# Optimization experiments

Measured on AMD Instinct MI355X. Metric: run time of the kernel, lower is better.

The kernel has to match this reference:

```python
import jax, jax.numpy as jnp
import numpy as np

B, LC, LE, H, V = 128, 256, 257, 512, 128
PAD = 0  # padding_token_index


def lstm_cell(x, h, c, Wih, Whh, b):
    # torch LSTMCell gate order: i, f, g, o
    g = x @ Wih.T + h @ Whh.T + b
    i, f, gg, o = jnp.split(g, 4, axis=-1)
    c = jax.nn.sigmoid(f) * c + jax.nn.sigmoid(i) * jnp.tanh(gg)
    h = jax.nn.sigmoid(o) * jnp.tanh(c)
    return h, c


def setup_inputs() -> dict:
    key = jax.random.key(0)
    ks = jax.random.split(key, 32)
    p = lambda k, shape: jax.random.normal(k, shape, jnp.float32) * 0.05
    d = {
        'C_idx': jax.random.randint(ks[0], (B, LC), 0, V, dtype=jnp.int32),
        'E_idx': jax.random.randint(ks[1], (B, LE), 0, V, dtype=jnp.int32),
        'C_pad': jnp.zeros((B, LC), dtype=bool),
        'enc_Wih_f': p(ks[2], (4 * H, V)),
        'enc_Whh_f': p(ks[3], (4 * H, H)),
        'enc_b_f': p(ks[4], (4 * H,)),
        'enc_Wih_b': p(ks[5], (4 * H, V)),
        'enc_Whh_b': p(ks[6], (4 * H, H)),
        'enc_b_b': p(ks[7], (4 * H,)),
        'dec_Wih': p(ks[8], (4 * H, H + V)),
        'dec_Whh': p(ks[9], (4 * H, H)),
        'dec_b': p(ks[10], (4 * H,)),
        'Wh': p(ks[11], (H, 2 * H)),
        'Wc': p(ks[12], (H, 2 * H)),
        'Wattn': p(ks[13], (H, 2 * H)),
        'Wout': p(ks[14], (H, 3 * H)),
        'Wvocab': p(ks[15], (V, H)),
        'pg_ctx': p(ks[16], (2 * H,)),
        'pg_in': p(ks[17], (V + H,)),
        'pg_h': p(ks[18], (H,)),
        'pg_c': p(ks[19], (H,)),
        'pg_b': p(ks[20], (1,)),
    }
    return d


def _forward(C_idx, E_idx, C_pad, enc_Wih_f, enc_Whh_f, enc_b_f, enc_Wih_b, enc_Whh_b, enc_b_b,
             dec_Wih, dec_Whh, dec_b, Wh, Wc, Wattn, Wout, Wvocab,
             pg_ctx, pg_in, pg_h, pg_c, pg_b):
    C = jax.nn.one_hot(C_idx, V, dtype=jnp.float32)      # [B,LC,V]
    E_emb = jax.nn.one_hot(E_idx, V, dtype=jnp.float32)  # [B,LE,V]
    z = jnp.zeros((B, H), jnp.float32)

    xs = jnp.swapaxes(C, 0, 1)  # [LC,B,V]

    def enc_fwd(carry, x):
        h, c = lstm_cell(x, carry[0], carry[1], enc_Wih_f, enc_Whh_f, enc_b_f)
        return (h, c), h

    def enc_bwd(carry, x):
        h, c = lstm_cell(x, carry[0], carry[1], enc_Wih_b, enc_Whh_b, enc_b_b)
        return (h, c), h

    (hf, cf), Hf = jax.lax.scan(enc_fwd, (z, z), xs)
    (hb, cb), Hb = jax.lax.scan(enc_bwd, (z, z), xs[::-1])
    Hb = Hb[::-1]
    enc = jnp.swapaxes(jnp.concatenate([Hf, Hb], axis=-1), 0, 1)  # [B,LC,2H]

    # decoder init state from final encoder states (fwd;bwd concat)
    h0 = jnp.concatenate([hf, hb], axis=-1) @ Wh.T
    c0 = jnp.concatenate([cf, cb], axis=-1) @ Wc.T

    enc_proj = enc @ Wattn.T  # [B,LC,H]

    def step(carry, x_emb):
        h, c, prev_out = carry
        nin = jnp.concatenate([x_emb, prev_out], axis=1)  # [B,V+H]
        h, c = lstm_cell(nin, h, c, dec_Wih, dec_Whh, dec_b)
        scores = jnp.einsum('blh,bh->bl', enc_proj, h)
        scores = jnp.where(C_pad, -jnp.inf, scores)
        attn = jax.nn.softmax(scores, axis=1)             # [B,LC]
        ctx = jnp.einsum('bl,blh->bh', attn, enc)         # [B,2H]
        t_out = jnp.tanh(jnp.concatenate([h, ctx], axis=1) @ Wout.T)  # [B,H]
        gen = jax.nn.softmax(t_out @ Wvocab.T, axis=1)    # [B,V]
        p_gen = jax.nn.sigmoid(ctx @ pg_ctx + nin @ pg_in + h @ pg_h + c @ pg_c + pg_b[0])[:, None]
        copy_p = attn * (1.0 - p_gen)
        out = jax.vmap(lambda o, idx, a: o.at[idx].add(a))(gen * p_gen, C_idx, copy_p)
        return (h, c, t_out), out

    xs2 = jnp.swapaxes(E_emb[:, :LE - 1], 0, 1)  # teacher inputs, step 0 = start token
    _, preds = jax.lax.scan(step, (h0, c0, z), xs2)
    preds = jnp.swapaxes(preds, 0, 1)  # [B,LE-1,V]

    tgt = E_idx[:, 1:]
    nll = -jnp.take_along_axis(jnp.log(preds), tgt[..., None], axis=2)[..., 0]
    return jnp.where(tgt == PAD, 0.0, nll)  # [B,LE-1], reduction='none'


def reference(C_idx, E_idx, C_pad, enc_Wih_f, enc_Whh_f, enc_b_f, enc_Wih_b, enc_Whh_b, enc_b_b,
              dec_Wih, dec_Whh, dec_b, Wh, Wc, Wattn, Wout, Wvocab,
              pg_ctx, pg_in, pg_h, pg_c, pg_b):
    return _forward(C_idx, E_idx, C_pad, enc_Wih_f, enc_Whh_f, enc_b_f, enc_Wih_b, enc_Whh_b, enc_b_b,
                    dec_Wih, dec_Whh, dec_b, Wh, Wc, Wattn, Wout, Wvocab,
                    pg_ctx, pg_in, pg_h, pg_c, pg_b)
```

## Files before the change

### kernel.cpp

```cpp
#include <hip/hip_runtime.h>

static constexpr size_t OFF_ENC   = 0;
static constexpr size_t OFF_WGE   = 67108864;
static constexpr size_t OFF_WIHTE = 71303168;
static constexpr size_t OFF_HENC  = 72351744;
static constexpr size_t OFF_CENC  = 72876032;
static constexpr size_t OFF_WGATE = 67108864;
static constexpr size_t OFF_XDEC  = 71303168;
static constexpr size_t OFF_WATTT = 71827456;
static constexpr size_t OFF_WOUT  = 72876032;
static constexpr size_t OFF_WVOCT = 74448896;
static constexpr size_t OFF_HDEC  = 74579968;
static constexpr size_t OFF_CDEC  = 74842112;
static constexpr size_t OFF_TOUT  = 75104256;
static constexpr size_t OFF_UFB   = 75366400;
static constexpr size_t OFF_CTXF  = 75628544;
static constexpr size_t OFF_CTXP  = 75890688;
static constexpr size_t OFF_SC    = 76414976;
static constexpr size_t OFF_MSP   = 76480512;
static constexpr size_t OFF_MD    = 76482560;

__device__ __forceinline__ float sigm(float x) { return 1.f / (1.f + expf(-x)); }
__device__ __forceinline__ unsigned short f2bf(float f) {
  unsigned u = __float_as_uint(f);
  u += 0x7fffu + ((u >> 16) & 1u);
  return (unsigned short)(u >> 16);
}
__device__ __forceinline__ float bfl(unsigned w) { return __uint_as_float(w << 16); }
__device__ __forceinline__ float bfh(unsigned w) { return __uint_as_float(w & 0xffff0000u); }
__device__ __forceinline__ float bf2f(unsigned short v) { return __uint_as_float(((unsigned)v) << 16); }

#if defined(__has_builtin)
#if __has_builtin(__builtin_amdgcn_fdot2_f32_bf16)
#define HAVE_DOT2BF 1
#endif
#endif
#ifdef HAVE_DOT2BF
typedef __bf16 bf2_t __attribute__((ext_vector_type(2)));
__device__ __forceinline__ float dot2bf(unsigned w, unsigned h, float acc) {
  return __builtin_amdgcn_fdot2_f32_bf16(__builtin_bit_cast(bf2_t, w),
                                         __builtin_bit_cast(bf2_t, h), acc, false);
}
#else
__device__ __forceinline__ float dot2bf(unsigned w, unsigned h, float acc) {
  return acc + bfl(w) * bfl(h) + bfh(w) * bfh(h);
}
#endif

__global__ __launch_bounds__(256) void k_pre1(const float* __restrict__ WhhF,
                                              const float* __restrict__ WhhB,
                                              const float* __restrict__ WihF,
                                              const float* __restrict__ WihB,
                                              char* __restrict__ wsb) {
  unsigned short* dst = (unsigned short*)(wsb + OFF_WGE);
  int id = blockIdx.x * 256 + threadIdx.x, str = gridDim.x * 256;
  for (int x = id; x < 2097152; x += str) {
    int dir = x >> 20, r = x & 1048575;
    int e = r & 7, j = (r >> 3) & 511, k2 = r >> 12;
    int g = e >> 1, k = k2 * 2 + (e & 1);
    const float* W = dir ? WhhB : WhhF;
    dst[x] = f2bf(W[((size_t)g * 512 + j) * 512 + k]);
  }
  for (int x = id; x < 524288; x += str) {
    int dir = x >> 18, r = x & 262143;
    int g = r & 3, j = (r >> 2) & 511, v = r >> 11;
    const float* W = dir ? WihB : WihF;
    dst[2097152 + x] = f2bf(W[((size_t)g * 512 + j) * 128 + v]);
  }
}

__global__ __launch_bounds__(512) void k_enc(const float* __restrict__ bF,
                                             const float* __restrict__ bB,
                                             const int* __restrict__ C_idx,
                                             char* __restrict__ wsb) {
  __shared__ __align__(16) unsigned short hbf[512];
  int bid = blockIdx.x;
  int b = bid & 127, dir = bid >> 7;
  int j = threadIdx.x;
  const unsigned short* WH = (const unsigned short*)(wsb + OFF_WGE) + (size_t)dir * 1048576;
  const unsigned short* WX = (const unsigned short*)(wsb + OFF_WGE) + 2097152 + (size_t)dir * 262144;
  const float* bias = dir ? bB : bF;
  float b0 = bias[j], b1 = bias[512 + j], b2 = bias[1024 + j], b3 = bias[1536 + j];
  unsigned short* encb = (unsigned short*)wsb + (size_t)b * 262144;
  const uint4* wp = (const uint4*)WH + j;
  float c = 0.f, h = 0.f;
  hbf[j] = 0;
  __syncthreads();
  for (int t = 0; t < 256; ++t) {
    int l = dir ? (255 - t) : t;
    int cidx = C_idx[b * 256 + l];
    uint2 xg = *(const uint2*)(WX + ((size_t)cidx * 512 + j) * 4);
    float a0 = b0 + bfl(xg.x), a1 = b1 + bfh(xg.x);
    float a2 = b2 + bfl(xg.y), a3 = b3 + bfh(xg.y);
    for (int k2 = 0; k2 < 256; ++k2) {
      uint4 w = wp[(size_t)k2 * 512];
      unsigned hp = *(const unsigned*)((const char*)hbf + k2 * 4);
      a0 = dot2bf(w.x, hp, a0);
      a1 = dot2bf(w.y, hp, a1);
      a2 = dot2bf(w.z, hp, a2);
      a3 = dot2bf(w.w, hp, a3);
    }
    float ig = sigm(a0), fg = sigm(a1), gg = tanhf(a2), og = sigm(a3);
    c = fg * c + ig * gg;
    h = og * tanhf(c);
    __syncthreads();
    unsigned short hb = f2bf(h);
    hbf[j] = hb;
    encb[(size_t)l * 1024 + dir * 512 + j] = hb;
    __syncthreads();
  }
  ((unsigned short*)(wsb + OFF_HENC))[(((size_t)(dir * 2 + 0) * 256 + (j >> 1)) * 128 + b) * 2 + (j & 1)] = f2bf(h);
  ((float*)(wsb + OFF_CENC))[((size_t)dir * 512 + j) * 128 + b] = c;
}

__global__ __launch_bounds__(512) void k_h0(const float* __restrict__ Wh,
                                            const float* __restrict__ Wc,
                                            char* __restrict__ wsb) {
  int tau = threadIdx.x;
  int b = tau & 127, slot = tau >> 7;
  int row = __builtin_amdgcn_readfirstlane(blockIdx.x * 4 + slot);
  int sel = row >> 9, j = row & 511;
  const float* W = (sel ? Wc : Wh) + (size_t)j * 1024;
  const unsigned short* HE = (const unsigned short*)(wsb + OFF_HENC);
  const float* CE = (const float*)(wsb + OFF_CENC);
  float acc = 0.f;
  for (int k = 0; k < 1024; ++k) {
    int dir = k >> 9, k5 = k & 511;
    float in;
    if (sel == 0)
      in = bf2f(HE[(((size_t)(dir * 2 + 0) * 256 + (k5 >> 1)) * 128 + b) * 2 + (k5 & 1)]);
    else
      in = CE[((size_t)dir * 512 + k5) * 128 + b];
    acc += W[k] * in;
  }
  if (sel == 0)
    ((unsigned short*)(wsb + OFF_HDEC))[(((size_t)(j >> 1)) * 128 + b) * 2 + (j & 1)] = f2bf(acc);
  else
    ((float*)(wsb + OFF_CDEC))[(size_t)j * 128 + b] = acc;
}

__global__ __launch_bounds__(256) void k_pre2(const float* __restrict__ dWih,
                                              const float* __restrict__ dWhh,
                                              const float* __restrict__ Wattn,
                                              const float* __restrict__ Wout,
                                              const float* __restrict__ Wvoc,
                                              char* __restrict__ wsb) {
  unsigned short* WG = (unsigned short*)(wsb + OFF_WGATE);
  unsigned short* XD = (unsigned short*)(wsb + OFF_XDEC);
  unsigned short* WA = (unsigned short*)(wsb + OFF_WATTT);
  unsigned short* WO = (unsigned short*)(wsb + OFF_WOUT);
  unsigned*       WV = (unsigned*)(wsb + OFF_WVOCT);
  int id = blockIdx.x * 256 + threadIdx.x, str = gridDim.x * 256;
  for (int x = id; x < 2048 * 1024; x += str) {
    int r = x >> 10, k = x & 1023;
    float v = (k < 512) ? dWih[(size_t)r * 640 + 128 + k] : dWhh[(size_t)r * 512 + (k - 512)];
    WG[x] = f2bf(v);
  }
  for (int x = id; x < 128 * 2048; x += str) {
    int v = x >> 11, r = x & 2047;
    XD[x] = f2bf(dWih[(size_t)r * 640 + v]);
  }
  for (int x = id; x < 1024 * 512; x += str) {
    int i = x >> 9, o = x & 511;
    WA[x] = f2bf(Wattn[(size_t)o * 1024 + i]);
  }
  for (int x = id; x < 512 * 1536; x += str) WO[x] = f2bf(Wout[x]);
  for (int x = id; x < 256 * 128; x += str) {
    int kk = x >> 7, v = x & 127;
    unsigned lo = f2bf(Wvoc[(size_t)v * 512 + 2 * kk]);
    unsigned hi = f2bf(Wvoc[(size_t)v * 512 + 2 * kk + 1]);
    WV[x] = lo | (hi << 16);
  }
}

__global__ __launch_bounds__(512) void k_gates(const int* __restrict__ E_idx,
                                               const float* __restrict__ db,
                                               char* __restrict__ wsb, int t) {
  __shared__ float part[2][4][128];
  int tau = threadIdx.x;
  int b = tau & 127, jslot = (tau >> 7) & 1, kh = tau >> 8;
  int j = __builtin_amdgcn_readfirstlane(blockIdx.x * 2 + jslot);
  int rp = t & 1, np = rp ^ 1;
  const unsigned* inw = (const unsigned*)(wsb + (kh ? OFF_HDEC : OFF_TOUT)) + (size_t)rp * 32768 + b;
  const unsigned* WG = (const unsigned*)(wsb + OFF_WGATE);
  const uint4* w0 = (const uint4*)(WG + (size_t)j * 512 + kh * 256);
  const uint4* w1 = (const uint4*)(WG + ((size_t)512 + j) * 512 + kh * 256);
  const uint4* w2 = (const uint4*)(WG + ((size_t)1024 + j) * 512 + kh * 256);
  const uint4* w3 = (const uint4*)(WG + ((size_t)1536 + j) * 512 + kh * 256);
  float a0 = 0.f, a1 = 0.f, a2 = 0.f, a3 = 0.f;
#pragma unroll 4
  for (int q = 0; q < 64; ++q) {
    uint4 W0 = w0[q], W1 = w1[q], W2 = w2[q], W3 = w3[q];
    unsigned i0 = inw[(q * 4 + 0) * 128], i1 = inw[(q * 4 + 1) * 128];
    unsigned i2 = inw[(q * 4 + 2) * 128], i3 = inw[(q * 4 + 3) * 128];
    a0 = dot2bf(W0.x, i0, a0); a0 = dot2bf(W0.y, i1, a0); a0 = dot2bf(W0.z, i2, a0); a0 = dot2bf(W0.w, i3, a0);
    a1 = dot2bf(W1.x, i0, a1); a1 = dot2bf(W1.y, i1, a1); a1 = dot2bf(W1.z, i2, a1); a1 = dot2bf(W1.w, i3, a1);
    a2 = dot2bf(W2.x, i0, a2); a2 = dot2bf(W2.y, i1, a2); a2 = dot2bf(W2.z, i2, a2); a2 = dot2bf(W2.w, i3, a2);
    a3 = dot2bf(W3.x, i0, a3); a3 = dot2bf(W3.y, i1, a3); a3 = dot2bf(W3.z, i2, a3); a3 = dot2bf(W3.w, i3, a3);
  }
  if (kh == 1) { part[jslot][0][b] = a0; part[jslot][1][b] = a1; part[jslot][2][b] = a2; part[jslot][3][b] = a3; }
  __syncthreads();
  if (kh == 0) {
    int xid = E_idx[b * 257 + t];
    const unsigned short* xg = (const unsigned short*)(wsb + OFF_XDEC) + (size_t)xid * 2048;
    float g0 = a0 + part[jslot][0][b] + db[j] + bf2f(xg[j]);
    float g1 = a1 + part[jslot][1][b] + db[512 + j] + bf2f(xg[512 + j]);
    float g2 = a2 + part[jslot][2][b] + db[1024 + j] + bf2f(xg[1024 + j]);
    float g3 = a3 + part[jslot][3][b] + db[1536 + j] + bf2f(xg[1536 + j]);
    float ig = sigm(g0), fg = sigm(g1), gg = tanhf(g2), og = sigm(g3);
    float* cp = (float*)(wsb + OFF_CDEC) + (size_t)j * 128 + b;
    float c = fg * (*cp) + ig * gg;
    *cp = c;
    float h = og * tanhf(c);
    ((unsigned short*)(wsb + OFF_HDEC))[(((size_t)np * 256 + (j >> 1)) * 128 + b) * 2 + (j & 1)] = f2bf(h);
  }
}

__global__ __launch_bounds__(512) void k_u(char* __restrict__ wsb, int t) {
  int tau = threadIdx.x;
  int b = tau & 127, slot = tau >> 7;
  int i = __builtin_amdgcn_readfirstlane(blockIdx.x * 4 + slot);
  int np = (t & 1) ^ 1;
  const unsigned* inw = (const unsigned*)(wsb + OFF_HDEC) + (size_t)np * 32768 + b;
  const uint4* w = (const uint4*)((const unsigned*)(wsb + OFF_WATTT) + (size_t)i * 256);
  float a = 0.f;
#pragma unroll 4
  for (int q = 0; q < 64; ++q) {
    uint4 W = w[q];
    a = dot2bf(W.x, inw[(q * 4 + 0) * 128], a);
    a = dot2bf(W.y, inw[(q * 4 + 1) * 128], a);
    a = dot2bf(W.z, inw[(q * 4 + 2) * 128], a);
    a = dot2bf(W.w, inw[(q * 4 + 3) * 128], a);
  }
  ((unsigned short*)(wsb + OFF_UFB))[(((size_t)(i >> 1)) * 128 + b) * 2 + (i & 1)] = f2bf(a);
}

__global__ __launch_bounds__(512) void k_attn1b(const unsigned char* __restrict__ C_pad,
                                                const int* __restrict__ E_idx,
                                                const float* __restrict__ pgc,
                                                const float* __restrict__ pgi,
                                                const float* __restrict__ pgh,
                                                const float* __restrict__ pgcc,
                                                const float* __restrict__ pgb,
                                                char* __restrict__ wsb, int t) {
  __shared__ __align__(16) unsigned short tile[32 * 1024];
  __shared__ __align__(16) unsigned ulds[512];
  __shared__ unsigned hlds[256];
  __shared__ float sc_l[32];
  __shared__ float p_l[32];
  __shared__ float red[16];
  int b = blockIdx.x, tau = threadIdx.x;
  int lane = tau & 63, wv = tau >> 6;
  int rp = t & 1, np = rp ^ 1;
  const unsigned* UW = (const unsigned*)(wsb + OFF_UFB) + b;
  ulds[tau] = UW[(size_t)tau * 128];
  if (tau < 256) hlds[tau] = ((const unsigned*)(wsb + OFF_HDEC))[(size_t)np * 32768 + (size_t)tau * 128 + b];
  float mold = -3.0e38f, ssum = 0.f, acc0 = 0.f, acc1 = 0.f;
  unsigned short* SCp = (unsigned short*)(wsb + OFF_SC) + (size_t)b * 256;
  for (int sub = 0; sub < 8; ++sub) {
    const uint4* src = (const uint4*)((const unsigned short*)wsb + ((size_t)b * 256 + sub * 32) * 1024);
    __syncthreads();
#pragma unroll
    for (int it = 0; it < 8; ++it) ((uint4*)tile)[it * 512 + tau] = src[it * 512 + tau];
    __syncthreads();
    const uint4* t4 = (const uint4*)tile;
    const uint4* u4 = (const uint4*)ulds;
    uint4 ua = u4[lane * 2], ub = u4[lane * 2 + 1];
#pragma unroll
    for (int li = 0; li < 4; ++li) {
      int l = wv * 4 + li;
      uint4 ea = t4[l * 128 + lane * 2];
      uint4 eb = t4[l * 128 + lane * 2 + 1];
      float s = 0.f;
      s = dot2bf(ea.x, ua.x, s); s = dot2bf(ea.y, ua.y, s);
      s = dot2bf(ea.z, ua.z, s); s = dot2bf(ea.w, ua.w, s);
      s = dot2bf(eb.x, ub.x, s); s = dot2bf(eb.y, ub.y, s);
      s = dot2bf(eb.z, ub.z, s); s = dot2bf(eb.w, ub.w, s);
      for (int o = 32; o; o >>= 1) s += __shfl_xor(s, o);
      if (lane == 0) {
        int gl = sub * 32 + l;
        if (C_pad[b * 256 + gl]) s = -3.0e38f;
        sc_l[l] = s;
        SCp[gl] = f2bf(s);
      }
    }
    __syncthreads();
    if (tau < 64) {
      float v = (tau < 32) ? sc_l[tau] : -3.0e38f;
      for (int o = 32; o; o >>= 1) v = fmaxf(v, __shfl_xor(v, o));
      if (tau == 0) red[0] = v;
    }
    __syncthreads();
    float mnew = fmaxf(mold, red[0]);
    float r = expf(mold - mnew);
    if (tau < 64) {
      float pv = (tau < 32) ? expf(sc_l[tau] - mnew) : 0.f;
      if (tau < 32) p_l[tau] = pv;
      for (int o = 32; o; o >>= 1) pv += __shfl_xor(pv, o);
      if (tau == 0) red[1] = pv;
    }
    __syncthreads();
    ssum = ssum * r + red[1];
    mold = mnew;
    acc0 *= r; acc1 *= r;
    const unsigned* tl = (const unsigned*)tile;
#pragma unroll 8
    for (int l = 0; l < 32; ++l) {
      float pv = p_l[l];
      unsigned ev = tl[l * 512 + tau];
      acc0 += pv * bfl(ev); acc1 += pv * bfh(ev);
    }
  }
  float invD = 1.f / ssum;
  float x0 = acc0 * invD, x1 = acc1 * invD;
  ((unsigned*)(wsb + OFF_CTXF))[(size_t)tau * 128 + b] =
      (unsigned)f2bf(x0) | ((unsigned)f2bf(x1) << 16);
  if (tau == 0) {
    float* MD = (float*)(wsb + OFF_MD);
    MD[b] = mold;
    MD[128 + b] = ssum;
  }
  float pp = x0 * pgc[2 * tau] + x1 * pgc[2 * tau + 1];
  {
    int f = tau;
    unsigned hw = hlds[f >> 1];
    float hv = (f & 1) ? bfh(hw) : bfl(hw);
    float cv = ((const float*)(wsb + OFF_CDEC))[(size_t)f * 128 + b];
    unsigned short tw = ((const unsigned short*)(wsb + OFF_TOUT))[(((size_t)rp * 256 + (f >> 1)) * 128 + b) * 2 + (f & 1)];
    pp += hv * pgh[f] + cv * pgcc[f] + bf2f(tw) * pgi[128 + f];
  }
  for (int o = 32; o; o >>= 1) pp += __shfl_xor(pp, o);
  if (lane == 0) red[8 + wv] = pp;
  __syncthreads();
  if (tau == 0) {
    float s = red[8] + red[9] + red[10] + red[11] + red[12] + red[13] + red[14] + red[15];
    s += pgi[E_idx[b * 257 + t]] + pgb[0];
    ((float*)(wsb + OFF_MD))[256 + b] = sigm(s);
  }
}

__global__ __launch_bounds__(512) void k_wout(char* __restrict__ wsb, int t) {
  __shared__ float part[2][128];
  int tau = threadIdx.x;
  int b = tau & 127, nslot = (tau >> 7) & 1, kh = tau >> 8;
  int n = __builtin_amdgcn_readfirstlane(blockIdx.x * 2 + nslot);
  int np = (t & 1) ^ 1;
  const unsigned* HW = (const unsigned*)(wsb + OFF_HDEC) + (size_t)np * 32768 + b;
  const unsigned* CW = (const unsigned*)(wsb + OFF_CTXF) + b;
  const unsigned* w = (const unsigned*)(wsb + OFF_WOUT) + (size_t)n * 768 + kh * 384;
  float a = 0.f;
  int p0 = kh * 384;
#pragma unroll 4
  for (int q = 0; q < 96; ++q) {
    uint4 W = ((const uint4*)w)[q];
#pragma unroll
    for (int e = 0; e < 4; ++e) {
      int pp = p0 + q * 4 + e;
      unsigned in = (pp < 256) ? HW[(size_t)pp * 128] : CW[(size_t)(pp - 256) * 128];
      unsigned wv = (e == 0) ? W.x : (e == 1) ? W.y : (e == 2) ? W.z : W.w;
      a = dot2bf(wv, in, a);
    }
  }
  if (kh == 1) part[nslot][b] = a;
  __syncthreads();
  if (kh == 0) {
    float tv = tanhf(a + part[nslot][b]);
    ((unsigned short*)(wsb + OFF_TOUT))[(((size_t)np * 256 + (n >> 1)) * 128 + b) * 2 + (n & 1)] = f2bf(tv);
  }
}

__global__ __launch_bounds__(256) void k_fin(const int* __restrict__ C_idx,
                                             const int* __restrict__ E_idx,
                                             char* __restrict__ wsb,
                                             float* __restrict__ out, int t) {
  __shared__ unsigned to_pld[256];
  __shared__ float lgp[2][128];
  __shared__ float lgf[128];
  __shared__ float red[8];
  int b = blockIdx.x, tau = threadIdx.x;
  int lane = tau & 63, wv = tau >> 6;
  int np = (t & 1) ^ 1;
  const unsigned* TOW = (const unsigned*)(wsb + OFF_TOUT) + (size_t)np * 32768 + b;
  to_pld[tau] = TOW[(size_t)tau * 128];
  __syncthreads();
  int v = tau & 127, kh = tau >> 7;
  const unsigned* WV = (const unsigned*)(wsb + OFF_WVOCT) + v;
  float a = 0.f;
#pragma unroll 8
  for (int kkk = 0; kkk < 128; ++kkk) {
    int kk = kh * 128 + kkk;
    a = dot2bf(WV[(size_t)kk * 128], to_pld[kk], a);
  }
  lgp[kh][v] = a;
  __syncthreads();
  if (tau < 128) {
    float lg = lgp[0][tau] + lgp[1][tau];
    lgf[tau] = lg;
    float m = lg;
    for (int o = 32; o; o >>= 1) m = fmaxf(m, __shfl_xor(m, o));
    if (lane == 0) red[wv] = m;
  }
  __syncthreads();
  float mx = fmaxf(red[0], red[1]);
  if (tau < 128) {
    float e = expf(lgf[tau] - mx);
    for (int o = 32; o; o >>= 1) e += __shfl_xor(e, o);
    if (lane == 0) red[2 + wv] = e;
  }
  __syncthreads();
  const float* MD = (const float*)(wsb + OFF_MD);
  float M = MD[b], D = MD[128 + b], pg = MD[256 + b];
  int tgt = E_idx[b * 257 + t + 1];
  float cm = 0.f;
  {
    float s = bf2f(((const unsigned short*)(wsb + OFF_SC))[(size_t)b * 256 + tau]);
    if (C_idx[b * 256 + tau] == tgt) cm = expf(s - M);
  }
  for (int o = 32; o; o >>= 1) cm += __shfl_xor(cm, o);
  if (lane == 0) red[4 + wv] = cm;
  __syncthreads();
  if (tau == 0) {
    float sume = red[2] + red[3];
    float copy_raw = red[4] + red[5] + red[6] + red[7];
    float gen_tgt = expf(lgf[tgt] - mx) / sume;
    float prob = pg * gen_tgt + (1.f - pg) * copy_raw / D;
    out[b * 256 + t] = (tgt == 0) ? 0.f : -logf(prob);
  }
}

extern "C" void kernel_launch(void* const* d_in, const int* in_sizes, int n_in,
                              void* d_out, int out_size, void* d_ws, size_t ws_size,
                              hipStream_t stream) {
  (void)in_sizes; (void)n_in; (void)out_size; (void)ws_size;
  const int* C_idx = (const int*)d_in[0];
  const int* E_idx = (const int*)d_in[1];
  const unsigned char* C_pad = (const unsigned char*)d_in[2];
  const float* eWihF = (const float*)d_in[3];
  const float* eWhhF = (const float*)d_in[4];
  const float* ebF   = (const float*)d_in[5];
  const float* eWihB = (const float*)d_in[6];
  const float* eWhhB = (const float*)d_in[7];
  const float* ebB   = (const float*)d_in[8];
  const float* dWih  = (const float*)d_in[9];
  const float* dWhh  = (const float*)d_in[10];
  const float* db    = (const float*)d_in[11];
  const float* Wh    = (const float*)d_in[12];
  const float* Wc    = (const float*)d_in[13];
  const float* Wattn = (const float*)d_in[14];
  const float* Wout  = (const float*)d_in[15];
  const float* Wvoc  = (const float*)d_in[16];
  const float* pgc   = (const float*)d_in[17];
  const float* pgi   = (const float*)d_in[18];
  const float* pgh   = (const float*)d_in[19];
  const float* pgcc  = (const float*)d_in[20];
  const float* pgb   = (const float*)d_in[21];
  char* wsb = (char*)d_ws;
  float* out = (float*)d_out;

  hipMemsetAsync(wsb + OFF_TOUT, 0, 262144, stream);

  k_pre1<<<256, 256, 0, stream>>>(eWhhF, eWhhB, eWihF, eWihB, wsb);
  k_enc<<<256, 512, 0, stream>>>(ebF, ebB, C_idx, wsb);
  k_h0<<<256, 512, 0, stream>>>(Wh, Wc, wsb);
  k_pre2<<<256, 256, 0, stream>>>(dWih, dWhh, Wattn, Wout, Wvoc, wsb);
  for (int t = 0; t < 256; ++t) {
    k_gates<<<256, 512, 0, stream>>>(E_idx, db, wsb, t);
    k_u<<<256, 512, 0, stream>>>(wsb, t);
    k_attn1b<<<128, 512, 0, stream>>>(C_pad, E_idx, pgc, pgi, pgh, pgcc, pgb, wsb, t);
    k_wout<<<256, 512, 0, stream>>>(wsb, t);
    k_fin<<<128, 256, 0, stream>>>(C_idx, E_idx, wsb, out, t);
  }
}
```

Before: 29.51 ms.

## Fuse decoder time loop into one persistent per-batch kernel

Replaces the 256-step host loop of five kernel launches (gates, attention projection, attention, output projection, final loss) with a single persistent kernel. Each of 128 blocks owns one batch row and iterates over all time steps, keeping h, c, context and scores in registers and LDS. Weights are repacked into k8-interleaved layouts so each thread reads uint4 weight chunks coalesced. This removes about 1280 launches and the global round-trips between them. The cost is using only 128 workgroups, with every block streaming the full decoder weights from L2 each step.

```diff
diff --git a/kernel.cpp b/kernel.cpp
--- a/kernel.cpp
+++ b/kernel.cpp
@@ -2,23 +2,15 @@
 
 static constexpr size_t OFF_ENC   = 0;
 static constexpr size_t OFF_WGE   = 67108864;
-static constexpr size_t OFF_WIHTE = 71303168;
 static constexpr size_t OFF_HENC  = 72351744;
 static constexpr size_t OFF_CENC  = 72876032;
-static constexpr size_t OFF_WGATE = 67108864;
+static constexpr size_t OFF_WGP   = 67108864;
 static constexpr size_t OFF_XDEC  = 71303168;
-static constexpr size_t OFF_WATTT = 71827456;
-static constexpr size_t OFF_WOUT  = 72876032;
-static constexpr size_t OFF_WVOCT = 74448896;
+static constexpr size_t OFF_WATTP = 71827456;
+static constexpr size_t OFF_WOUTP = 72876032;
+static constexpr size_t OFF_WVOCP = 74448896;
 static constexpr size_t OFF_HDEC  = 74579968;
 static constexpr size_t OFF_CDEC  = 74842112;
-static constexpr size_t OFF_TOUT  = 75104256;
-static constexpr size_t OFF_UFB   = 75366400;
-static constexpr size_t OFF_CTXF  = 75628544;
-static constexpr size_t OFF_CTXP  = 75890688;
-static constexpr size_t OFF_SC    = 76414976;
-static constexpr size_t OFF_MSP   = 76480512;
-static constexpr size_t OFF_MD    = 76482560;
 
 __device__ __forceinline__ float sigm(float x) { return 1.f / (1.f + expf(-x)); }
 __device__ __forceinline__ unsigned short f2bf(float f) {
@@ -29,6 +21,9 @@
 __device__ __forceinline__ float bfl(unsigned w) { return __uint_as_float(w << 16); }
 __device__ __forceinline__ float bfh(unsigned w) { return __uint_as_float(w & 0xffff0000u); }
 __device__ __forceinline__ float bf2f(unsigned short v) { return __uint_as_float(((unsigned)v) << 16); }
+__device__ __forceinline__ unsigned packbf(float lo, float hi) {
+  return (unsigned)f2bf(lo) | ((unsigned)f2bf(hi) << 16);
+}
 
 #if defined(__has_builtin)
 #if __has_builtin(__builtin_amdgcn_fdot2_f32_bf16)
@@ -46,6 +41,11 @@
   return acc + bfl(w) * bfl(h) + bfh(w) * bfh(h);
 }
 #endif
+__device__ __forceinline__ float dot4q(uint4 W, uint4 I, float a) {
+  a = dot2bf(W.x, I.x, a); a = dot2bf(W.y, I.y, a);
+  a = dot2bf(W.z, I.z, a); a = dot2bf(W.w, I.w, a);
+  return a;
+}
 
 __global__ __launch_bounds__(256) void k_pre1(const float* __restrict__ WhhF,
                                               const float* __restrict__ WhhB,
@@ -139,292 +139,255 @@
     ((float*)(wsb + OFF_CDEC))[(size_t)j * 128 + b] = acc;
 }
 
-__global__ __launch_bounds__(256) void k_pre2(const float* __restrict__ dWih,
-                                              const float* __restrict__ dWhh,
-                                              const float* __restrict__ Wattn,
-                                              const float* __restrict__ Wout,
-                                              const float* __restrict__ Wvoc,
-                                              char* __restrict__ wsb) {
-  unsigned short* WG = (unsigned short*)(wsb + OFF_WGATE);
+__global__ __launch_bounds__(256) void k_pre2p(const float* __restrict__ dWih,
+                                               const float* __restrict__ dWhh,
+                                               const float* __restrict__ Wattn,
+                                               const float* __restrict__ Wout,
+                                               const float* __restrict__ Wvoc,
+                                               char* __restrict__ wsb) {
+  unsigned* WG = (unsigned*)(wsb + OFF_WGP);
   unsigned short* XD = (unsigned short*)(wsb + OFF_XDEC);
-  unsigned short* WA = (unsigned short*)(wsb + OFF_WATTT);
-  unsigned short* WO = (unsigned short*)(wsb + OFF_WOUT);
-  unsigned*       WV = (unsigned*)(wsb + OFF_WVOCT);
+  unsigned* WA = (unsigned*)(wsb + OFF_WATTP);
+  unsigned* WO = (unsigned*)(wsb + OFF_WOUTP);
+  unsigned* WV = (unsigned*)(wsb + OFF_WVOCP);
   int id = blockIdx.x * 256 + threadIdx.x, str = gridDim.x * 256;
-  for (int x = id; x < 2048 * 1024; x += str) {
-    int r = x >> 10, k = x & 1023;
-    float v = (k < 512) ? dWih[(size_t)r * 640 + 128 + k] : dWhh[(size_t)r * 512 + (k - 512)];
-    WG[x] = f2bf(v);
+  for (int x = id; x < 1048576; x += str) {
+    int j = x & 3, r = (x >> 2) & 2047, k8 = x >> 13;
+    int d0 = k8 * 8 + 2 * j;
+    float v0 = (d0 < 512) ? dWih[(size_t)r * 640 + 128 + d0] : dWhh[(size_t)r * 512 + (d0 - 512)];
+    int d1 = d0 + 1;
+    float v1 = (d1 < 512) ? dWih[(size_t)r * 640 + 128 + d1] : dWhh[(size_t)r * 512 + (d1 - 512)];
+    WG[x] = packbf(v0, v1);
   }
   for (int x = id; x < 128 * 2048; x += str) {
     int v = x >> 11, r = x & 2047;
     XD[x] = f2bf(dWih[(size_t)r * 640 + v]);
   }
-  for (int x = id; x < 1024 * 512; x += str) {
-    int i = x >> 9, o = x & 511;
-    WA[x] = f2bf(Wattn[(size_t)o * 1024 + i]);
-  }
-  for (int x = id; x < 512 * 1536; x += str) WO[x] = f2bf(Wout[x]);
-  for (int x = id; x < 256 * 128; x += str) {
-    int kk = x >> 7, v = x & 127;
-    unsigned lo = f2bf(Wvoc[(size_t)v * 512 + 2 * kk]);
-    unsigned hi = f2bf(Wvoc[(size_t)v * 512 + 2 * kk + 1]);
-    WV[x] = lo | (hi << 16);
-  }
-}
-
-__global__ __launch_bounds__(512) void k_gates(const int* __restrict__ E_idx,
-                                               const float* __restrict__ db,
-                                               char* __restrict__ wsb, int t) {
-  __shared__ float part[2][4][128];
-  int tau = threadIdx.x;
-  int b = tau & 127, jslot = (tau >> 7) & 1, kh = tau >> 8;
-  int j = __builtin_amdgcn_readfirstlane(blockIdx.x * 2 + jslot);
-  int rp = t & 1, np = rp ^ 1;
-  const unsigned* inw = (const unsigned*)(wsb + (kh ? OFF_HDEC : OFF_TOUT)) + (size_t)rp * 32768 + b;
-  const unsigned* WG = (const unsigned*)(wsb + OFF_WGATE);
-  const uint4* w0 = (const uint4*)(WG + (size_t)j * 512 + kh * 256);
-  const uint4* w1 = (const uint4*)(WG + ((size_t)512 + j) * 512 + kh * 256);
-  const uint4* w2 = (const uint4*)(WG + ((size_t)1024 + j) * 512 + kh * 256);
-  const uint4* w3 = (const uint4*)(WG + ((size_t)1536 + j) * 512 + kh * 256);
-  float a0 = 0.f, a1 = 0.f, a2 = 0.f, a3 = 0.f;
-#pragma unroll 4
-  for (int q = 0; q < 64; ++q) {
-    uint4 W0 = w0[q], W1 = w1[q], W2 = w2[q], W3 = w3[q];
-    unsigned i0 = inw[(q * 4 + 0) * 128], i1 = inw[(q * 4 + 1) * 128];
-    unsigned i2 = inw[(q * 4 + 2) * 128], i3 = inw[(q * 4 + 3) * 128];
-    a0 = dot2bf(W0.x, i0, a0); a0 = dot2bf(W0.y, i1, a0); a0 = dot2bf(W0.z, i2, a0); a0 = dot2bf(W0.w, i3, a0);
-    a1 = dot2bf(W1.x, i0, a1); a1 = dot2bf(W1.y, i1, a1); a1 = dot2bf(W1.z, i2, a1); a1 = dot2bf(W1.w, i3, a1);
-    a2 = dot2bf(W2.x, i0, a2); a2 = dot2bf(W2.y, i1, a2); a2 = dot2bf(W2.z, i2, a2); a2 = dot2bf(W2.w, i3, a2);
-    a3 = dot2bf(W3.x, i0, a3); a3 = dot2bf(W3.y, i1, a3); a3 = dot2bf(W3.z, i2, a3); a3 = dot2bf(W3.w, i3, a3);
-  }
-  if (kh == 1) { part[jslot][0][b] = a0; part[jslot][1][b] = a1; part[jslot][2][b] = a2; part[jslot][3][b] = a3; }
-  __syncthreads();
-  if (kh == 0) {
-    int xid = E_idx[b * 257 + t];
-    const unsigned short* xg = (const unsigned short*)(wsb + OFF_XDEC) + (size_t)xid * 2048;
-    float g0 = a0 + part[jslot][0][b] + db[j] + bf2f(xg[j]);
-    float g1 = a1 + part[jslot][1][b] + db[512 + j] + bf2f(xg[512 + j]);
-    float g2 = a2 + part[jslot][2][b] + db[1024 + j] + bf2f(xg[1024 + j]);
-    float g3 = a3 + part[jslot][3][b] + db[1536 + j] + bf2f(xg[1536 + j]);
-    float ig = sigm(g0), fg = sigm(g1), gg = tanhf(g2), og = sigm(g3);
-    float* cp = (float*)(wsb + OFF_CDEC) + (size_t)j * 128 + b;
-    float c = fg * (*cp) + ig * gg;
-    *cp = c;
-    float h = og * tanhf(c);
-    ((unsigned short*)(wsb + OFF_HDEC))[(((size_t)np * 256 + (j >> 1)) * 128 + b) * 2 + (j & 1)] = f2bf(h);
-  }
-}
-
-__global__ __launch_bounds__(512) void k_u(char* __restrict__ wsb, int t) {
-  int tau = threadIdx.x;
-  int b = tau & 127, slot = tau >> 7;
-  int i = __builtin_amdgcn_readfirstlane(blockIdx.x * 4 + slot);
-  int np = (t & 1) ^ 1;
-  const unsigned* inw = (const unsigned*)(wsb + OFF_HDEC) + (size_t)np * 32768 + b;
-  const uint4* w = (const uint4*)((const unsigned*)(wsb + OFF_WATTT) + (size_t)i * 256);
-  float a = 0.f;
-#pragma unroll 4
-  for (int q = 0; q < 64; ++q) {
-    uint4 W = w[q];
-    a = dot2bf(W.x, inw[(q * 4 + 0) * 128], a);
-    a = dot2bf(W.y, inw[(q * 4 + 1) * 128], a);
-    a = dot2bf(W.z, inw[(q * 4 + 2) * 128], a);
-    a = dot2bf(W.w, inw[(q * 4 + 3) * 128], a);
-  }
-  ((unsigned short*)(wsb + OFF_UFB))[(((size_t)(i >> 1)) * 128 + b) * 2 + (i & 1)] = f2bf(a);
-}
-
-__global__ __launch_bounds__(512) void k_attn1b(const unsigned char* __restrict__ C_pad,
-                                                const int* __restrict__ E_idx,
-                                                const float* __restrict__ pgc,
-                                                const float* __restrict__ pgi,
-                                                const float* __restrict__ pgh,
-                                                const float* __restrict__ pgcc,
-                                                const float* __restrict__ pgb,
-                                                char* __restrict__ wsb, int t) {
+  for (int x = id; x < 262144; x += str) {
+    int j = x & 3, i = (x >> 2) & 1023, o8 = x >> 12;
+    int o0 = o8 * 8 + 2 * j;
+    WA[x] = packbf(Wattn[(size_t)o0 * 1024 + i], Wattn[(size_t)(o0 + 1) * 1024 + i]);
+  }
+  for (int x = id; x < 393216; x += str) {
+    int j = x & 3, n = (x >> 2) & 511, k8 = x >> 11;
+    int d0 = k8 * 8 + 2 * j;
+    WO[x] = packbf(Wout[(size_t)n * 1536 + d0], Wout[(size_t)n * 1536 + d0 + 1]);
+  }
+  for (int x = id; x < 32768; x += str) {
+    int j = x & 3, v = (x >> 2) & 127, k8 = x >> 9;
+    int d0 = k8 * 8 + 2 * j;
+    WV[x] = packbf(Wvoc[(size_t)v * 512 + d0], Wvoc[(size_t)v * 512 + d0 + 1]);
+  }
+}
+
+__global__ __launch_bounds__(512) void k_dec(const int* __restrict__ C_idx,
+                                             const int* __restrict__ E_idx,
+                                             const unsigned char* __restrict__ C_pad,
+                                             const float* __restrict__ db,
+                                             const float* __restrict__ pgc,
+                                             const float* __restrict__ pgi,
+                                             const float* __restrict__ pgh,
+                                             const float* __restrict__ pgcc,
+                                             const float* __restrict__ pgb,
+                                             char* __restrict__ wsb,
+                                             float* __restrict__ out) {
   __shared__ __align__(16) unsigned short tile[32 * 1024];
+  __shared__ __align__(16) unsigned in8[512];
   __shared__ __align__(16) unsigned ulds[512];
-  __shared__ unsigned hlds[256];
+  __shared__ __align__(16) unsigned ctxp[512];
+  __shared__ float scf[256];
   __shared__ float sc_l[32];
   __shared__ float p_l[32];
   __shared__ float red[16];
+  __shared__ float lgp[4][128];
+  __shared__ float lgf[128];
+  __shared__ float mdl[4];
+  __shared__ int eix[257];
+  __shared__ int ci[256];
+  __shared__ unsigned char cpad[256];
+
   int b = blockIdx.x, tau = threadIdx.x;
   int lane = tau & 63, wv = tau >> 6;
-  int rp = t & 1, np = rp ^ 1;
-  const unsigned* UW = (const unsigned*)(wsb + OFF_UFB) + b;
-  ulds[tau] = UW[(size_t)tau * 128];
-  if (tau < 256) hlds[tau] = ((const unsigned*)(wsb + OFF_HDEC))[(size_t)np * 32768 + (size_t)tau * 128 + b];
-  float mold = -3.0e38f, ssum = 0.f, acc0 = 0.f, acc1 = 0.f;
-  unsigned short* SCp = (unsigned short*)(wsb + OFF_SC) + (size_t)b * 256;
-  for (int sub = 0; sub < 8; ++sub) {
-    const uint4* src = (const uint4*)((const unsigned short*)wsb + ((size_t)b * 256 + sub * 32) * 1024);
-    __syncthreads();
+
+  const uint4* WG4 = (const uint4*)(wsb + OFF_WGP);
+  const unsigned short* XD = (const unsigned short*)(wsb + OFF_XDEC);
+  const uint4* WA4 = (const uint4*)(wsb + OFF_WATTP);
+  const uint4* WO4 = (const uint4*)(wsb + OFF_WOUTP);
+  const uint4* WV4 = (const uint4*)(wsb + OFF_WVOCP);
+  const unsigned short* encB = (const unsigned short*)wsb + (size_t)b * 262144;
+
+  if (tau < 256) {
+    ci[tau] = C_idx[b * 256 + tau];
+    cpad[tau] = C_pad[b * 256 + tau];
+    in8[tau] = 0;
+    in8[256 + tau] = ((const unsigned*)(wsb + OFF_HDEC))[(size_t)tau * 128 + b];
+  }
+  if (tau < 257) eix[tau] = E_idx[b * 257 + tau];
+  float c = ((const float*)(wsb + OFF_CDEC))[(size_t)tau * 128 + b];
+  float db0 = db[tau], db1 = db[512 + tau], db2 = db[1024 + tau], db3 = db[1536 + tau];
+  float pgc0 = pgc[2 * tau], pgc1 = pgc[2 * tau + 1];
+  float pghr = pgh[tau], pgcr = pgcc[tau], pgir = pgi[128 + tau];
+  float pgb0 = pgb[0];
+  __syncthreads();
+
+  const uint4* in4 = (const uint4*)in8;
+  const uint4* ctx4 = (const uint4*)ctxp;
+  const uint4* u4 = (const uint4*)ulds;
+  const uint4* t4 = (const uint4*)tile;
+  const unsigned* tl = (const unsigned*)tile;
+
+  for (int t = 0; t < 256; ++t) {
+    int xid = eix[t], tgt = eix[t + 1];
+    const unsigned short* xg = XD + (size_t)xid * 2048;
+    float a0 = db0 + bf2f(xg[tau]);
+    float a1 = db1 + bf2f(xg[512 + tau]);
+    float a2 = db2 + bf2f(xg[1024 + tau]);
+    float a3 = db3 + bf2f(xg[1536 + tau]);
+#pragma unroll 2
+    for (int k8 = 0; k8 < 128; ++k8) {
+      uint4 iv = in4[k8];
+      const uint4* wp = WG4 + (size_t)k8 * 2048;
+      a0 = dot4q(wp[tau], iv, a0);
+      a1 = dot4q(wp[512 + tau], iv, a1);
+      a2 = dot4q(wp[1024 + tau], iv, a2);
+      a3 = dot4q(wp[1536 + tau], iv, a3);
+    }
+    float ig = sigm(a0), fg = sigm(a1), gg = tanhf(a2), og = sigm(a3);
+    c = fg * c + ig * gg;
+    float h = og * tanhf(c);
+    __syncthreads();
+    ((unsigned short*)in8)[512 + tau] = f2bf(h);
+    __syncthreads();
+    float ua = 0.f, ub = 0.f;
+#pragma unroll 4
+    for (int o8 = 0; o8 < 64; ++o8) {
+      uint4 hv = in4[64 + o8];
+      const uint4* wp = WA4 + (size_t)o8 * 1024;
+      ua = dot4q(wp[tau], hv, ua);
+      ub = dot4q(wp[512 + tau], hv, ub);
+    }
+    ((unsigned short*)ulds)[tau] = f2bf(ua);
+    ((unsigned short*)ulds)[512 + tau] = f2bf(ub);
+    float mold = -3.0e38f, ssum = 0.f, acc0 = 0.f, acc1 = 0.f;
+    for (int sub = 0; sub < 8; ++sub) {
+      const uint4* src = (const uint4*)encB + (size_t)sub * 4096;
+      __syncthreads();
 #pragma unroll
-    for (int it = 0; it < 8; ++it) ((uint4*)tile)[it * 512 + tau] = src[it * 512 + tau];
-    __syncthreads();
-    const uint4* t4 = (const uint4*)tile;
-    const uint4* u4 = (const uint4*)ulds;
-    uint4 ua = u4[lane * 2], ub = u4[lane * 2 + 1];
+      for (int it = 0; it < 8; ++it) ((uint4*)tile)[it * 512 + tau] = src[it * 512 + tau];
+      __syncthreads();
+      uint4 uaV = u4[lane * 2], ubV = u4[lane * 2 + 1];
 #pragma unroll
-    for (int li = 0; li < 4; ++li) {
-      int l = wv * 4 + li;
-      uint4 ea = t4[l * 128 + lane * 2];
-      uint4 eb = t4[l * 128 + lane * 2 + 1];
-      float s = 0.f;
-      s = dot2bf(ea.x, ua.x, s); s = dot2bf(ea.y, ua.y, s);
-      s = dot2bf(ea.z, ua.z, s); s = dot2bf(ea.w, ua.w, s);
-      s = dot2bf(eb.x, ub.x, s); s = dot2bf(eb.y, ub.y, s);
-      s = dot2bf(eb.z, ub.z, s); s = dot2bf(eb.w, ub.w, s);
-      for (int o = 32; o; o >>= 1) s += __shfl_xor(s, o);
-      if (lane == 0) {
-        int gl = sub * 32 + l;
-        if (C_pad[b * 256 + gl]) s = -3.0e38f;
-        sc_l[l] = s;
-        SCp[gl] = f2bf(s);
+      for (int li = 0; li < 4; ++li) {
+        int l = wv * 4 + li;
+        uint4 ea = t4[l * 128 + lane * 2];
+        uint4 eb = t4[l * 128 + lane * 2 + 1];
+        float s = 0.f;
+        s = dot4q(ea, uaV, s);
+        s = dot4q(eb, ubV, s);
+        for (int o = 32; o; o >>= 1) s += __shfl_xor(s, o);
+        if (lane == 0) {
+          int gl = sub * 32 + l;
+          if (cpad[gl]) s = -3.0e38f;
+          sc_l[l] = s;
+          scf[gl] = s;
+        }
       }
-    }
-    __syncthreads();
-    if (tau < 64) {
-      float v = (tau < 32) ? sc_l[tau] : -3.0e38f;
-      for (int o = 32; o; o >>= 1) v = fmaxf(v, __shfl_xor(v, o));
-      if (tau == 0) red[0] = v;
-    }
-    __syncthreads();
-    float mnew = fmaxf(mold, red[0]);
-    float r = expf(mold - mnew);
-    if (tau < 64) {
-      float pv = (tau < 32) ? expf(sc_l[tau] - mnew) : 0.f;
-      if (tau < 32) p_l[tau] = pv;
-      for (int o = 32; o; o >>= 1) pv += __shfl_xor(pv, o);
-      if (tau == 0) red[1] = pv;
-    }
-    __syncthreads();
-    ssum = ssum * r + red[1];
-    mold = mnew;
-    acc0 *= r; acc1 *= r;
-    const unsigned* tl = (const unsigned*)tile;
+      __syncthreads();
+      if (tau < 64) {
+        float v = (tau < 32) ? sc_l[tau] : -3.0e38f;
+        for (int o = 32; o; o >>= 1) v = fmaxf(v, __shfl_xor(v, o));
+        if (tau == 0) red[0] = v;
+      }
+      __syncthreads();
+      float mnew = fmaxf(mold, red[0]);
+      float r = expf(mold - mnew);
+      if (tau < 64) {
+        float pv = (tau < 32) ? expf(sc_l[tau] - mnew) : 0.f;
+        if (tau < 32) p_l[tau] = pv;
+        for (int o = 32; o; o >>= 1) pv += __shfl_xor(pv, o);
+        if (tau == 0) red[1] = pv;
+      }
+      __syncthreads();
+      ssum = ssum * r + red[1];
+      mold = mnew;
+      acc0 *= r; acc1 *= r;
 #pragma unroll 8
-    for (int l = 0; l < 32; ++l) {
-      float pv = p_l[l];
-      unsigned ev = tl[l * 512 + tau];
-      acc0 += pv * bfl(ev); acc1 += pv * bfh(ev);
-    }
-  }
-  float invD = 1.f / ssum;
-  float x0 = acc0 * invD, x1 = acc1 * invD;
-  ((unsigned*)(wsb + OFF_CTXF))[(size_t)tau * 128 + b] =
-      (unsigned)f2bf(x0) | ((unsigned)f2bf(x1) << 16);
-  if (tau == 0) {
-    float* MD = (float*)(wsb + OFF_MD);
-    MD[b] = mold;
-    MD[128 + b] = ssum;
-  }
-  float pp = x0 * pgc[2 * tau] + x1 * pgc[2 * tau + 1];
-  {
-    int f = tau;
-    unsigned hw = hlds[f >> 1];
-    float hv = (f & 1) ? bfh(hw) : bfl(hw);
-    float cv = ((const float*)(wsb + OFF_CDEC))[(size_t)f * 128 + b];
-    unsigned short tw = ((const unsigned short*)(wsb + OFF_TOUT))[(((size_t)rp * 256 + (f >> 1)) * 128 + b) * 2 + (f & 1)];
-    pp += hv * pgh[f] + cv * pgcc[f] + bf2f(tw) * pgi[128 + f];
-  }
-  for (int o = 32; o; o >>= 1) pp += __shfl_xor(pp, o);
-  if (lane == 0) red[8 + wv] = pp;
-  __syncthreads();
-  if (tau == 0) {
-    float s = red[8] + red[9] + red[10] + red[11] + red[12] + red[13] + red[14] + red[15];
-    s += pgi[E_idx[b * 257 + t]] + pgb[0];
-    ((float*)(wsb + OFF_MD))[256 + b] = sigm(s);
-  }
-}
-
-__global__ __launch_bounds__(512) void k_wout(char* __restrict__ wsb, int t) {
-  __shared__ float part[2][128];
-  int tau = threadIdx.x;
-  int b = tau & 127, nslot = (tau >> 7) & 1, kh = tau >> 8;
-  int n = __builtin_amdgcn_readfirstlane(blockIdx.x * 2 + nslot);
-  int np = (t & 1) ^ 1;
-  const unsigned* HW = (const unsigned*)(wsb + OFF_HDEC) + (size_t)np * 32768 + b;
-  const unsigned* CW = (const unsigned*)(wsb + OFF_CTXF) + b;
-  const unsigned* w = (const unsigned*)(wsb + OFF_WOUT) + (size_t)n * 768 + kh * 384;
-  float a = 0.f;
-  int p0 = kh * 384;
-#pragma unroll 4
-  for (int q = 0; q < 96; ++q) {
-    uint4 W = ((const uint4*)w)[q];
+      for (int l = 0; l < 32; ++l) {
+        float pv = p_l[l];
+        unsigned ev = tl[l * 512 + tau];
+        acc0 += pv * bfl(ev); acc1 += pv * bfh(ev);
+      }
+    }
+    float invD = 1.f / ssum;
+    float x0 = acc0 * invD, x1 = acc1 * invD;
+    ctxp[tau] = packbf(x0, x1);
+    float pp = x0 * pgc0 + x1 * pgc1;
+    {
+      unsigned hw = in8[256 + (tau >> 1)];
+      float hv = (tau & 1) ? bfh(hw) : bfl(hw);
+      unsigned tw = in8[tau >> 1];
+      float tv = (tau & 1) ? bfh(tw) : bfl(tw);
+      pp += hv * pghr + c * pgcr + tv * pgir;
+    }
+    for (int o = 32; o; o >>= 1) pp += __shfl_xor(pp, o);
+    if (lane == 0) red[8 + wv] = pp;
+    __syncthreads();
+    if (tau == 0) {
+      float s = red[8] + red[9] + red[10] + red[11] + red[12] + red[13] + red[14] + red[15];
+      s += pgi[xid] + pgb0;
+      mdl[0] = sigm(s);
+    }
+    float aw = 0.f;
+#pragma unroll 2
+    for (int k8 = 0; k8 < 192; ++k8) {
+      uint4 iv = (k8 < 64) ? in4[64 + k8] : ctx4[k8 - 64];
+      aw = dot4q((WO4 + (size_t)k8 * 512)[tau], iv, aw);
+    }
+    float tv2 = tanhf(aw);
+    __syncthreads();
+    ((unsigned short*)in8)[tau] = f2bf(tv2);
+    __syncthreads();
+    {
+      int v = tau & 127, seg = tau >> 7;
+      float af = 0.f;
 #pragma unroll
-    for (int e = 0; e < 4; ++e) {
-      int pp = p0 + q * 4 + e;
-      unsigned in = (pp < 256) ? HW[(size_t)pp * 128] : CW[(size_t)(pp - 256) * 128];
-      unsigned wv = (e == 0) ? W.x : (e == 1) ? W.y : (e == 2) ? W.z : W.w;
-      a = dot2bf(wv, in, a);
-    }
-  }
-  if (kh == 1) part[nslot][b] = a;
-  __syncthreads();
-  if (kh == 0) {
-    float tv = tanhf(a + part[nslot][b]);
-    ((unsigned short*)(wsb + OFF_TOUT))[(((size_t)np * 256 + (n >> 1)) * 128 + b) * 2 + (n & 1)] = f2bf(tv);
-  }
-}
-
-__global__ __launch_bounds__(256) void k_fin(const int* __restrict__ C_idx,
-                                             const int* __restrict__ E_idx,
-                                             char* __restrict__ wsb,
-                                             float* __restrict__ out, int t) {
-  __shared__ unsigned to_pld[256];
-  __shared__ float lgp[2][128];
-  __shared__ float lgf[128];
-  __shared__ float red[8];
-  int b = blockIdx.x, tau = threadIdx.x;
-  int lane = tau & 63, wv = tau >> 6;
-  int np = (t & 1) ^ 1;
-  const unsigned* TOW = (const unsigned*)(wsb + OFF_TOUT) + (size_t)np * 32768 + b;
-  to_pld[tau] = TOW[(size_t)tau * 128];
-  __syncthreads();
-  int v = tau & 127, kh = tau >> 7;
-  const unsigned* WV = (const unsigned*)(wsb + OFF_WVOCT) + v;
-  float a = 0.f;
-#pragma unroll 8
-  for (int kkk = 0; kkk < 128; ++kkk) {
-    int kk = kh * 128 + kkk;
-    a = dot2bf(WV[(size_t)kk * 128], to_pld[kk], a);
-  }
-  lgp[kh][v] = a;
-  __syncthreads();
-  if (tau < 128) {
-    float lg = lgp[0][tau] + lgp[1][tau];
-    lgf[tau] = lg;
-    float m = lg;
-    for (int o = 32; o; o >>= 1) m = fmaxf(m, __shfl_xor(m, o));
-    if (lane == 0) red[wv] = m;
-  }
-  __syncthreads();
-  float mx = fmaxf(red[0], red[1]);
-  if (tau < 128) {
-    float e = expf(lgf[tau] - mx);
-    for (int o = 32; o; o >>= 1) e += __shfl_xor(e, o);
-    if (lane == 0) red[2 + wv] = e;
-  }
-  __syncthreads();
-  const float* MD = (const float*)(wsb + OFF_MD);
-  float M = MD[b], D = MD[128 + b], pg = MD[256 + b];
-  int tgt = E_idx[b * 257 + t + 1];
-  float cm = 0.f;
-  {
-    float s = bf2f(((const unsigned short*)(wsb + OFF_SC))[(size_t)b * 256 + tau]);
-    if (C_idx[b * 256 + tau] == tgt) cm = expf(s - M);
-  }
-  for (int o = 32; o; o >>= 1) cm += __shfl_xor(cm, o);
-  if (lane == 0) red[4 + wv] = cm;
-  __syncthreads();
-  if (tau == 0) {
-    float sume = red[2] + red[3];
-    float copy_raw = red[4] + red[5] + red[6] + red[7];
-    float gen_tgt = expf(lgf[tgt] - mx) / sume;
-    float prob = pg * gen_tgt + (1.f - pg) * copy_raw / D;
-    out[b * 256 + t] = (tgt == 0) ? 0.f : -logf(prob);
+      for (int q = 0; q < 16; ++q) {
+        int k8 = seg * 16 + q;
+        af = dot4q((WV4 + (size_t)k8 * 128)[v], in4[k8], af);
+      }
+      lgp[seg][v] = af;
+    }
+    __syncthreads();
+    if (tau < 128) {
+      float lg = lgp[0][tau] + lgp[1][tau] + lgp[2][tau] + lgp[3][tau];
+      lgf[tau] = lg;
+      float m = lg;
+      for (int o = 32; o; o >>= 1) m = fmaxf(m, __shfl_xor(m, o));
+      if (lane == 0) red[wv] = m;
+    }
+    __syncthreads();
+    float mx = fmaxf(red[0], red[1]);
+    if (tau < 128) {
+      float e = expf(lgf[tau] - mx);
+      for (int o = 32; o; o >>= 1) e += __shfl_xor(e, o);
+      if (lane == 0) red[2 + wv] = e;
+    }
+    float cm = 0.f;
+    if (tau < 256) {
+      if (ci[tau] == tgt) cm = expf(scf[tau] - mold);
+    }
+    for (int o = 32; o; o >>= 1) cm += __shfl_xor(cm, o);
+    if (lane == 0 && wv < 4) red[4 + wv] = cm;
+    __syncthreads();
+    if (tau == 0) {
+      float sume = red[2] + red[3];
+      float copy_raw = (red[4] + red[5] + red[6] + red[7]) / ssum;
+      float gen_tgt = expf(lgf[tgt] - mx) / sume;
+      float pg = mdl[0];
+      float prob = pg * gen_tgt + (1.f - pg) * copy_raw;
+      out[b * 256 + t] = (tgt == 0) ? 0.f : -logf(prob);
+    }
+    __syncthreads();
   }
 }
 
@@ -457,17 +420,9 @@
   char* wsb = (char*)d_ws;
   float* out = (float*)d_out;
 
-  hipMemsetAsync(wsb + OFF_TOUT, 0, 262144, stream);
-
   k_pre1<<<256, 256, 0, stream>>>(eWhhF, eWhhB, eWihF, eWihB, wsb);
   k_enc<<<256, 512, 0, stream>>>(ebF, ebB, C_idx, wsb);
   k_h0<<<256, 512, 0, stream>>>(Wh, Wc, wsb);
-  k_pre2<<<256, 256, 0, stream>>>(dWih, dWhh, Wattn, Wout, Wvoc, wsb);
-  for (int t = 0; t < 256; ++t) {
-    k_gates<<<256, 512, 0, stream>>>(E_idx, db, wsb, t);
-    k_u<<<256, 512, 0, stream>>>(wsb, t);
-    k_attn1b<<<128, 512, 0, stream>>>(C_pad, E_idx, pgc, pgi, pgh, pgcc, pgb, wsb, t);
-    k_wout<<<256, 512, 0, stream>>>(wsb, t);
-    k_fin<<<128, 256, 0, stream>>>(C_idx, E_idx, wsb, out, t);
-  }
-}
+  k_pre2p<<<256, 256, 0, stream>>>(dWih, dWhh, Wattn, Wout, Wvoc, wsb);
+  k_dec<<<128, 512, 0, stream>>>(C_idx, E_idx, C_pad, db, pgc, pgi, pgh, pgcc, pgb, wsb, out);
+}
```

Result: slower. 65.08 ms (+120.5%).
